# Performance work log

Measured on AMD Instinct MI355X. Metric: run time of the kernel, lower is better.

The kernel has to match this reference:

```python
import jax, jax.numpy as jnp
import numpy as np

B, S, IN, OUT, H, M = 16, 512, 512, 512, 8, 4
HF = OUT // H  # head_feats = 64


def setup_inputs() -> dict:
    key = jax.random.key(0)
    ks = jax.random.split(key, 12)
    std = 0.02
    queries = jax.random.normal(ks[0], (B, S, IN), jnp.float32)
    keys = jax.random.normal(ks[1], (B, S, IN), jnp.float32)
    timespans = jax.random.uniform(ks[2], (B, S), jnp.float32)
    # causal mask tiled over heads*batch, matching [H*B, S, S] score shape
    attention_masks = jnp.broadcast_to(jnp.tril(jnp.ones((S, S), jnp.float32)), (H * B, S, S))
    event_marks = jax.random.uniform(ks[3], (H * B, 1, S, M), jnp.float32)
    Wq = std * jax.random.normal(ks[4], (IN, OUT), jnp.float32)
    Wk = std * jax.random.normal(ks[5], (IN, OUT), jnp.float32)
    Wv = std * jax.random.normal(ks[6], (IN, OUT), jnp.float32)
    Wt = std * jax.random.normal(ks[7], (IN, OUT), jnp.float32)
    Wi = std * jax.random.normal(ks[8], (HF + 1, M * HF), jnp.float32)  # fc_i weight
    bi = jnp.zeros((M * HF,), jnp.float32)                               # fc_i bias
    weight_i = std * jax.random.normal(ks[9], (M, HF), jnp.float32)
    scale_i = jnp.zeros((M,), jnp.float32)
    return {"queries": queries, "keys": keys, "timespans": timespans,
            "attention_masks": attention_masks, "event_marks": event_marks,
            "Wq": Wq, "Wk": Wk, "Wv": Wv, "Wt": Wt, "Wi": Wi, "bi": bi,
            "weight_i": weight_i, "scale_i": scale_i}


def reference(queries, keys, timespans, attention_masks, event_marks,
              Wq, Wk, Wv, Wt, Wi, bi, weight_i, scale_i):
    # torch's cat(chunk(X, H, dim=2), dim=0) == [B,S,H,HF] -> [H,B,S,HF] -> flat h*B+b
    def split_heads(X):
        return X.reshape(B, S, H, HF).transpose(2, 0, 1, 3)  # [H,B,S,HF]

    Q = split_heads(queries @ Wq)
    K = split_heads(keys @ Wk)
    V = split_heads(keys @ Wv)
    T = split_heads(keys @ Wt)

    scores = jnp.einsum('hbqf,hbkf->hbqk', Q, K) / jnp.sqrt(jnp.float32(OUT))
    mask = attention_masks.reshape(H, B, S, S)
    scores = jnp.where(mask == 0.0, jnp.float32(-2 ** 32 + 1), scores)
    attn = jax.nn.softmax(scores, axis=-1)  # [H,B,Sq,Sk]

    E = jnp.einsum('hbqk,hbkf->hbqf', attn, T)  # events fed to intensity net

    # --- Hawkes intensities ---
    ts = jnp.broadcast_to(timespans[None, :, :, None], (H, B, S, 1))
    mu = jax.nn.sigmoid(jnp.concatenate([E, ts], axis=-1) @ Wi + bi)  # [H,B,S,M*HF]
    mu = mu.reshape(H, B, S, M, HF)  # chunk over marks along feature dim
    scale = jnp.exp(scale_i)  # [M]
    lam = jnp.einsum('hbsmf,mf->hbsm', mu, weight_i) / scale
    lam = scale * jnp.log1p(jnp.exp(lam))  # scaled softplus, [H,B,S,M]

    # mark_inty[h,b,q,k] = sum_m lam[h,b,q,m] * event_marks[h,b,k,m]
    em = event_marks.reshape(H, B, S, M)
    mark_inty = jnp.einsum('hbqm,hbkm->hbqk', lam, em)

    out = jnp.einsum('hbqk,hbkf->hbqf', attn * mark_inty, V)
    out = out.transpose(1, 2, 0, 3).reshape(B, S, OUT) + queries[..., :OUT]
    all_mark_inty = lam.reshape(H * B, S, M)
    return out, all_mark_inty
```

## Files before the change

### kernel.cpp

```cpp
#include <hip/hip_runtime.h>
#include <math.h>

typedef __attribute__((ext_vector_type(8))) short short8;
typedef __attribute__((ext_vector_type(4))) float f32x4;

static __device__ __forceinline__ unsigned short f2bf(float f) {
  unsigned int u = __float_as_uint(f);
  u += 0x7FFFu + ((u >> 16) & 1u);
  return (unsigned short)(u >> 16);
}

static __device__ __forceinline__ void cp16(void* lds, const void* g) {
  __builtin_amdgcn_global_load_lds((const __attribute__((address_space(1))) void*)g,
                                   (__attribute__((address_space(3))) void*)lds,
                                   16, 0, 0);
}

__global__ __launch_bounds__(256) void convert_k(
    const float* __restrict__ qin, const float* __restrict__ kin,
    const float* __restrict__ Wq, const float* __restrict__ Wk,
    const float* __restrict__ Wv, const float* __restrict__ Wt,
    const float* __restrict__ Wi,
    unsigned short* __restrict__ qbf, unsigned short* __restrict__ kbf,
    unsigned short* __restrict__ Wb, unsigned short* __restrict__ WiF)
{
  __shared__ unsigned short tr[64 * 68];
  const int blk = blockIdx.x, tid = threadIdx.x;
  if (blk < 8192) {
    const float* src = (blk < 4096) ? qin : kin;
    unsigned short* dst = (blk < 4096) ? qbf : kbf;
    int i = ((blk & 4095) * 256 + tid) * 4;
    float4 v = *(const float4*)(src + i);
    ushort4 o;
    o.x = f2bf(v.x); o.y = f2bf(v.y); o.z = f2bf(v.z); o.w = f2bf(v.w);
    *(ushort4*)(dst + i) = o;
  } else if (blk < 8448) {
    int t = blk - 8192;
    int which = t >> 6, tile = t & 63;
    int r0 = (tile >> 3) << 6, c0 = (tile & 7) << 6;
    const float* W = (which == 0) ? Wq : (which == 1) ? Wk : (which == 2) ? Wv : Wt;
    const int rr = tid >> 4, cc = (tid & 15) << 2;
#pragma unroll
    for (int u = 0; u < 4; ++u) {
      int r = rr + u * 16;
      float4 v = *(const float4*)(W + (size_t)(r0 + r) * 512 + c0 + cc);
      tr[(cc + 0) * 68 + r] = f2bf(v.x);
      tr[(cc + 1) * 68 + r] = f2bf(v.y);
      tr[(cc + 2) * 68 + r] = f2bf(v.z);
      tr[(cc + 3) * 68 + r] = f2bf(v.w);
    }
    __syncthreads();
    unsigned short* dst = Wb + which * 262144;
#pragma unroll
    for (int u = 0; u < 4; ++u) {
      int c = rr + u * 16;
      ushort4 o = *(const ushort4*)&tr[c * 68 + cc];
      *(ushort4*)(dst + (size_t)(c0 + c) * 512 + r0 + cc) = o;
    }
  } else {
    int e = (blk - 8448) * 256 + tid;
    int j = e & 7, ll = (e >> 3) & 63, r = e >> 9;
    int kk = r % 3, nt = r / 3;
    int col = nt * 16 + (ll & 15);
    int k = kk * 32 + (ll >> 4) * 8 + j;
    float val = (k < 64) ? Wi[k * 256 + col] : ((k == 64) ? Wi[16384 + col] : 0.0f);
    WiF[e] = f2bf(val);
  }
}

__global__ __launch_bounds__(256) void proj_mfma(
    const unsigned short* __restrict__ qin_bf, const unsigned short* __restrict__ kin_bf,
    const unsigned short* __restrict__ Wb,
    unsigned short* __restrict__ Qg, unsigned short* __restrict__ Kg,
    unsigned short* __restrict__ Vt, unsigned short* __restrict__ Tt)
{
  const int which = blockIdx.z;
  const unsigned short* A = (which == 0) ? qin_bf : kin_bf;
  const unsigned short* W = Wb + which * 262144;
  const int row0 = blockIdx.x * 128;
  const int col0 = blockIdx.y * 128;
  const int tid = threadIdx.x;
  const int wv = tid >> 6, l = tid & 63;
  const int quad = l >> 4, lc = l & 15;
  const int wm = wv >> 1, wn = wv & 1;

  __shared__ unsigned short Asm[128 * 32];
  __shared__ unsigned short Bsm[128 * 32];

  f32x4 acc[4][4] = {};
  const int c0 = tid, c1 = tid + 256;

  for (int k0 = 0; k0 < 512; k0 += 32) {
    __syncthreads();
    cp16(&Asm[c0 * 8], A + (size_t)(row0 + (c0 >> 2)) * 512 + k0 + (c0 & 3) * 8);
    cp16(&Asm[c1 * 8], A + (size_t)(row0 + (c1 >> 2)) * 512 + k0 + (c1 & 3) * 8);
    cp16(&Bsm[c0 * 8], W + (size_t)(col0 + (c0 >> 2)) * 512 + k0 + (c0 & 3) * 8);
    cp16(&Bsm[c1 * 8], W + (size_t)(col0 + (c1 >> 2)) * 512 + k0 + (c1 & 3) * 8);
    __syncthreads();
    short8 a[4], b[4];
#pragma unroll
    for (int mi = 0; mi < 4; ++mi)
      a[mi] = *(const short8*)&Asm[(wm * 64 + mi * 16 + lc) * 32 + quad * 8];
#pragma unroll
    for (int nj = 0; nj < 4; ++nj)
      b[nj] = *(const short8*)&Bsm[(wn * 64 + nj * 16 + lc) * 32 + quad * 8];
#pragma unroll
    for (int mi = 0; mi < 4; ++mi)
#pragma unroll
      for (int nj = 0; nj < 4; ++nj)
        acc[mi][nj] = __builtin_amdgcn_mfma_f32_16x16x32_bf16(a[mi], b[nj], acc[mi][nj], 0, 0, 0);
  }

  const int h = (col0 >> 6) + wn;
  const int bidx = row0 >> 9;
  const int hb = h * 16 + bidx;
  if (which < 2) {
    unsigned short* C = (which == 0) ? Qg : Kg;
    const float os = (which == 0) ? 0.044194173824159216f : 1.0f;
#pragma unroll
    for (int mi = 0; mi < 4; ++mi) {
      int sbase = (row0 & 511) + wm * 64 + mi * 16 + quad * 4;
#pragma unroll
      for (int nj = 0; nj < 4; ++nj) {
        size_t base = (size_t)hb * 32768 + (size_t)sbase * 64 + nj * 16 + lc;
#pragma unroll
        for (int reg = 0; reg < 4; ++reg)
          C[base + (size_t)reg * 64] = f2bf(acc[mi][nj][reg] * os);
      }
    }
  } else {
    unsigned short* C = (which == 2) ? Vt : Tt;
    unsigned short* scr = wn ? Bsm : Asm;
    const int sb = (row0 & 511) + wm * 64;
    __syncthreads();
#pragma unroll
    for (int round = 0; round < 2; ++round) {
      if (wm == round) {
#pragma unroll
        for (int mi = 0; mi < 4; ++mi)
#pragma unroll
          for (int nj = 0; nj < 4; ++nj)
#pragma unroll
            for (int reg = 0; reg < 4; ++reg) {
              int f = nj * 16 + lc, s = mi * 16 + quad * 4 + reg;
              int g = (s >> 3) ^ (f & 7);
              scr[f * 64 + g * 8 + (s & 7)] = f2bf(acc[mi][nj][reg]);
            }
#pragma unroll
        for (int it = 0; it < 8; ++it) {
          int fl = it * 8 + (l >> 3);
          int gg = (l & 7) ^ (fl & 7);
          short8 v = *(const short8*)&scr[fl * 64 + gg * 8];
          *(short8*)(C + (size_t)hb * 32768 + (size_t)fl * 512 + sb + (l & 7) * 8) = v;
        }
      }
      __syncthreads();
    }
  }
}

__global__ __launch_bounds__(256, 2) void attn_fused(
    const unsigned short* __restrict__ Qg, const unsigned short* __restrict__ Kg,
    const unsigned short* __restrict__ Vtg, const unsigned short* __restrict__ Ttg,
    const unsigned short* __restrict__ WiF,
    const float* __restrict__ bi, const float* __restrict__ wim,
    const float* __restrict__ sci, const float* __restrict__ tsp,
    const float* __restrict__ em, const float* __restrict__ queries,
    float* __restrict__ out, float* __restrict__ lamout)
{
  const int hb = blockIdx.x;
  const int y = blockIdx.y;
  const int qb = (y == 0) ? 3 : (y == 1) ? 2 : (y == 2) ? 0 : 1;
  const int q0 = qb << 7;
  const int kts = 2 * qb + 2;
  const int tid = threadIdx.x, wv = tid >> 6, l = tid & 63;
  const int quad = l >> 4, lc = l & 15;
  const int xg = lc & 7;

  __shared__ unsigned short Qs[8192];
  __shared__ unsigned short Ks[2][4096];
  __shared__ unsigned short TVs[2][4096];
  __shared__ unsigned short Wl[4][3072];
  __shared__ float emS[2][256];

  const int e1 = tid + 256;
  const int sr0 = tid >> 3, sg0 = (tid & 7) ^ (sr0 & 7);
  const int sr1 = e1 >> 3,  sg1 = (e1 & 7) ^ (sr1 & 7);
  const int sqk0 = sr0 * 64 + sg0 * 8,  sqk1 = sr1 * 64 + sg1 * 8;
  const int stv0 = sr0 * 512 + sg0 * 8, stv1 = sr1 * 512 + sg1 * 8;

  const unsigned short* KgB = Kg + (size_t)hb * 32768;
  const unsigned short* TgB = Ttg + (size_t)hb * 32768;
  const unsigned short* VgB = Vtg + (size_t)hb * 32768;

  const unsigned short* Qbase = Qg + (size_t)hb * 32768 + q0 * 64;
#pragma unroll
  for (int u = 0; u < 4; ++u) {
    int e = tid + u * 256;
    int r = e >> 3, g = (e & 7) ^ (r & 7);
    cp16(&Qs[e * 8], Qbase + r * 64 + g * 8);
  }
  cp16(&Ks[0][tid * 8], KgB + sqk0);
  cp16(&Ks[0][e1 * 8], KgB + sqk1);
  cp16(&TVs[0][tid * 8], TgB + stv0);
  cp16(&TVs[0][e1 * 8], TgB + stv1);
  __syncthreads();

  short8 aq[2][2];
#pragma unroll
  for (int rt = 0; rt < 2; ++rt)
#pragma unroll
    for (int kk = 0; kk < 2; ++kk)
      aq[rt][kk] = *(const short8*)&Qs[(wv * 32 + rt * 16 + lc) * 64 + ((kk * 4 + quad) ^ xg) * 8];

  f32x4 Eacc[2][4] = {};
  float lsum[2][4] = {};

  for (int kt = 0; kt < kts; ++kt) {
    const int cur = kt & 1, nxt = cur ^ 1;
    const int k0 = kt << 6;
    if (kt + 1 < kts) {
      const int k1 = (kt + 1) << 6;
      cp16(&Ks[nxt][tid * 8], KgB + k1 * 64 + sqk0);
      cp16(&Ks[nxt][e1 * 8], KgB + k1 * 64 + sqk1);
      cp16(&TVs[nxt][tid * 8], TgB + k1 + stv0);
      cp16(&TVs[nxt][e1 * 8], TgB + k1 + stv1);
    }
    f32x4 sc[2][4] = {};
#pragma unroll
    for (int kk = 0; kk < 2; ++kk)
#pragma unroll
      for (int nj = 0; nj < 4; ++nj) {
        short8 b = *(const short8*)&Ks[cur][(nj * 16 + lc) * 64 + ((kk * 4 + quad) ^ xg) * 8];
        sc[0][nj] = __builtin_amdgcn_mfma_f32_16x16x32_bf16(aq[0][kk], b, sc[0][nj], 0, 0, 0);
        sc[1][nj] = __builtin_amdgcn_mfma_f32_16x16x32_bf16(aq[1][kk], b, sc[1][nj], 0, 0, 0);
      }
#pragma unroll
    for (int rt = 0; rt < 2; ++rt) {
      const int gq = q0 + wv * 32 + rt * 16 + quad * 4;
#pragma unroll
      for (int nj = 0; nj < 4; ++nj) {
        int col = nj * 16 + lc;
#pragma unroll
        for (int reg = 0; reg < 4; ++reg) {
          float pv = __expf(sc[rt][nj][reg]);
          if (k0 + col > gq + reg) pv = 0.0f;
          lsum[rt][reg] += pv;
          int row = rt * 16 + quad * 4 + reg;
          int gp = (nj * 2 + (lc >> 3)) ^ (row & 7);
          Wl[wv][row * 96 + gp * 8 + (lc & 7)] = f2bf(pv);
        }
      }
    }
#pragma unroll
    for (int rt = 0; rt < 2; ++rt)
#pragma unroll
      for (int kk = 0; kk < 2; ++kk) {
        short8 a = *(const short8*)&Wl[wv][(rt * 16 + lc) * 96 + ((kk * 4 + quad) ^ xg) * 8];
#pragma unroll
        for (int fj = 0; fj < 4; ++fj) {
          short8 b = *(const short8*)&TVs[cur][(fj * 16 + lc) * 64 + ((kk * 4 + quad) ^ xg) * 8];
          Eacc[rt][fj] = __builtin_amdgcn_mfma_f32_16x16x32_bf16(a, b, Eacc[rt][fj], 0, 0, 0);
        }
      }
    __syncthreads();
  }

  float inv[2][4];
#pragma unroll
  for (int rt = 0; rt < 2; ++rt)
#pragma unroll
    for (int reg = 0; reg < 4; ++reg) {
      float s = lsum[rt][reg];
#pragma unroll
      for (int off = 1; off < 16; off <<= 1) s += __shfl_xor(s, off);
      inv[rt][reg] = 1.0f / s;
    }

#pragma unroll
  for (int rt = 0; rt < 2; ++rt)
#pragma unroll
    for (int reg = 0; reg < 4; ++reg) {
      int row = rt * 16 + quad * 4 + reg;
      int gq = q0 + wv * 32 + rt * 16 + quad * 4;
      unsigned short* rp = &Wl[wv][row * 96];
#pragma unroll
      for (int fj = 0; fj < 4; ++fj) {
        int gp = (fj * 2 + (lc >> 3)) ^ (row & 7);
        rp[gp * 8 + (lc & 7)] = f2bf(Eacc[rt][fj][reg] * inv[rt][reg]);
      }
      float tsv = (lc == 0) ? tsp[(hb & 15) * 512 + gq + reg] : 0.0f;
      int gt = 8 + ((lc >> 3) ^ (row & 3));
      rp[gt * 8 + (lc & 7)] = f2bf(tsv);
      int gz = 8 + ((2 + (lc >> 3)) ^ (row & 3));
      rp[gz * 8 + (lc & 7)] = 0;
    }

  float lam4[2][4][4];
#pragma unroll
  for (int rt = 0; rt < 2; ++rt) {
    short8 ia[3];
    ia[0] = *(const short8*)&Wl[wv][(rt * 16 + lc) * 96 + ((0 + quad) ^ xg) * 8];
    ia[1] = *(const short8*)&Wl[wv][(rt * 16 + lc) * 96 + ((4 + quad) ^ xg) * 8];
    ia[2] = *(const short8*)&Wl[wv][(rt * 16 + lc) * 96 + (8 + (quad ^ (lc & 3))) * 8];
    float lac[4][4] = {};
#pragma unroll
    for (int nt = 0; nt < 16; ++nt) {
      f32x4 iacc = {};
#pragma unroll
      for (int kk = 0; kk < 3; ++kk) {
        short8 b = *(const short8*)(WiF + ((nt * 3 + kk) * 64 + l) * 8);
        iacc = __builtin_amdgcn_mfma_f32_16x16x32_bf16(ia[kk], b, iacc, 0, 0, 0);
      }
      float bvv = bi[nt * 16 + lc];
      float wmv = wim[nt * 16 + lc];
#pragma unroll
      for (int reg = 0; reg < 4; ++reg) {
        float mu = 1.0f / (1.0f + __expf(-(iacc[reg] + bvv)));
        lac[reg][nt >> 2] += mu * wmv;
      }
    }
#pragma unroll
    for (int m = 0; m < 4; ++m) {
      float scv = __expf(sci[m]);
#pragma unroll
      for (int reg = 0; reg < 4; ++reg) {
        float s = lac[reg][m];
#pragma unroll
        for (int off = 1; off < 16; off <<= 1) s += __shfl_xor(s, off);
        float z = s / scv;
        float sp = (z > 20.0f) ? z : log1pf(__expf(z));
        lam4[rt][reg][m] = scv * sp;
      }
    }
    if (lc < 4) {
      int gq = q0 + wv * 32 + rt * 16 + quad * 4;
#pragma unroll
      for (int reg = 0; reg < 4; ++reg) {
        float v = (lc == 0) ? lam4[rt][reg][0] : (lc == 1) ? lam4[rt][reg][1]
                : (lc == 2) ? lam4[rt][reg][2] : lam4[rt][reg][3];
        lamout[((size_t)hb * 512 + gq + reg) * 4 + lc] = v;
      }
    }
#pragma unroll
    for (int reg = 0; reg < 4; ++reg)
#pragma unroll
      for (int m = 0; m < 4; ++m)
        lam4[rt][reg][m] *= inv[rt][reg];
  }

  cp16(&Ks[0][tid * 8], KgB + sqk0);
  cp16(&Ks[0][e1 * 8], KgB + sqk1);
  cp16(&TVs[0][tid * 8], VgB + stv0);
  cp16(&TVs[0][e1 * 8], VgB + stv1);
  emS[0][tid] = em[(size_t)hb * 2048 + tid];
  __syncthreads();

  f32x4 Oacc[2][4] = {};
  for (int kt = 0; kt < kts; ++kt) {
    const int cur = kt & 1, nxt = cur ^ 1;
    const int k0 = kt << 6;
    if (kt + 1 < kts) {
      const int k1 = (kt + 1) << 6;
      cp16(&Ks[nxt][tid * 8], KgB + k1 * 64 + sqk0);
      cp16(&Ks[nxt][e1 * 8], KgB + k1 * 64 + sqk1);
      cp16(&TVs[nxt][tid * 8], VgB + k1 + stv0);
      cp16(&TVs[nxt][e1 * 8], VgB + k1 + stv1);
      emS[nxt][tid] = em[(size_t)hb * 2048 + k1 * 4 + tid];
    }
    f32x4 sc[2][4] = {};
#pragma unroll
    for (int kk = 0; kk < 2; ++kk)
#pragma unroll
      for (int nj = 0; nj < 4; ++nj) {
        short8 b = *(const short8*)&Ks[cur][(nj * 16 + lc) * 64 + ((kk * 4 + quad) ^ xg) * 8];
        sc[0][nj] = __builtin_amdgcn_mfma_f32_16x16x32_bf16(aq[0][kk], b, sc[0][nj], 0, 0, 0);
        sc[1][nj] = __builtin_amdgcn_mfma_f32_16x16x32_bf16(aq[1][kk], b, sc[1][nj], 0, 0, 0);
      }
#pragma unroll
    for (int rt = 0; rt < 2; ++rt) {
      const int gq = q0 + wv * 32 + rt * 16 + quad * 4;
#pragma unroll
      for (int nj = 0; nj < 4; ++nj) {
        int col = nj * 16 + lc;
        float4 emv = *(const float4*)&emS[cur][col * 4];
#pragma unroll
        for (int reg = 0; reg < 4; ++reg) {
          float pv = __expf(sc[rt][nj][reg]);
          if (k0 + col > gq + reg) pv = 0.0f;
          float mk = lam4[rt][reg][0] * emv.x + lam4[rt][reg][1] * emv.y +
                     lam4[rt][reg][2] * emv.z + lam4[rt][reg][3] * emv.w;
          int row = rt * 16 + quad * 4 + reg;
          int gp = (nj * 2 + (lc >> 3)) ^ (row & 7);
          Wl[wv][row * 96 + gp * 8 + (lc & 7)] = f2bf(pv * mk);
        }
      }
    }
#pragma unroll
    for (int rt = 0; rt < 2; ++rt)
#pragma unroll
      for (int kk = 0; kk < 2; ++kk) {
        short8 a = *(const short8*)&Wl[wv][(rt * 16 + lc) * 96 + ((kk * 4 + quad) ^ xg) * 8];
#pragma unroll
        for (int fj = 0; fj < 4; ++fj) {
          short8 b = *(const short8*)&TVs[cur][(fj * 16 + lc) * 64 + ((kk * 4 + quad) ^ xg) * 8];
          Oacc[rt][fj] = __builtin_amdgcn_mfma_f32_16x16x32_bf16(a, b, Oacc[rt][fj], 0, 0, 0);
        }
      }
    __syncthreads();
  }

  const int h = hb >> 4, bidx = hb & 15;
#pragma unroll
  for (int rt = 0; rt < 2; ++rt) {
    const int gq = q0 + wv * 32 + rt * 16 + quad * 4;
#pragma unroll
    for (int reg = 0; reg < 4; ++reg) {
      size_t o = (size_t)bidx * 262144 + (size_t)(gq + reg) * 512 + h * 64 + lc;
#pragma unroll
      for (int fj = 0; fj < 4; ++fj)
        out[o + fj * 16] = Oacc[rt][fj][reg] + queries[o + fj * 16];
    }
  }
}

extern "C" void kernel_launch(void* const* d_in, const int* in_sizes, int n_in,
                              void* d_out, int out_size, void* d_ws, size_t ws_size,
                              hipStream_t stream)
{
  (void)in_sizes; (void)n_in; (void)out_size; (void)ws_size;
  const float* queries = (const float*)d_in[0];
  const float* keys    = (const float*)d_in[1];
  const float* tsp     = (const float*)d_in[2];
  const float* em      = (const float*)d_in[4];
  const float* Wq      = (const float*)d_in[5];
  const float* Wk      = (const float*)d_in[6];
  const float* Wv      = (const float*)d_in[7];
  const float* Wt      = (const float*)d_in[8];
  const float* Wi      = (const float*)d_in[9];
  const float* bi      = (const float*)d_in[10];
  const float* wim     = (const float*)d_in[11];
  const float* sci     = (const float*)d_in[12];
  float* out = (float*)d_out;

  char* w = (char*)d_ws;
  unsigned short* Qg     = (unsigned short*)(w + 0);
  unsigned short* Kg     = (unsigned short*)(w + 8388608);
  unsigned short* Vt     = (unsigned short*)(w + 16777216);
  unsigned short* Tt     = (unsigned short*)(w + 25165824);
  unsigned short* qin_bf = (unsigned short*)(w + 33554432);
  unsigned short* kin_bf = (unsigned short*)(w + 41943040);
  unsigned short* Wb     = (unsigned short*)(w + 50331648);
  unsigned short* WiF    = (unsigned short*)(w + 52428800);

  convert_k<<<8544, 256, 0, stream>>>(queries, keys, Wq, Wk, Wv, Wt, Wi,
                                      qin_bf, kin_bf, Wb, WiF);
  proj_mfma<<<dim3(64, 4, 4), 256, 0, stream>>>(qin_bf, kin_bf, Wb, Qg, Kg, Vt, Tt);
  attn_fused<<<dim3(128, 4), 256, 0, stream>>>(Qg, Kg, Vt, Tt, WiF, bi, wim, sci,
                                               tsp, em, queries, out,
                                               out + 4194304);
}
```

Measured before the change: 313.1 us.

## Fuse input bf16 conversion into projection GEMM and cache softmax probabilities in registers

```diff
diff --git a/kernel.cpp b/kernel.cpp
--- a/kernel.cpp
+++ b/kernel.cpp
@@ -17,26 +17,15 @@
 }
 
 __global__ __launch_bounds__(256) void convert_k(
-    const float* __restrict__ qin, const float* __restrict__ kin,
     const float* __restrict__ Wq, const float* __restrict__ Wk,
     const float* __restrict__ Wv, const float* __restrict__ Wt,
     const float* __restrict__ Wi,
-    unsigned short* __restrict__ qbf, unsigned short* __restrict__ kbf,
     unsigned short* __restrict__ Wb, unsigned short* __restrict__ WiF)
 {
   __shared__ unsigned short tr[64 * 68];
   const int blk = blockIdx.x, tid = threadIdx.x;
-  if (blk < 8192) {
-    const float* src = (blk < 4096) ? qin : kin;
-    unsigned short* dst = (blk < 4096) ? qbf : kbf;
-    int i = ((blk & 4095) * 256 + tid) * 4;
-    float4 v = *(const float4*)(src + i);
-    ushort4 o;
-    o.x = f2bf(v.x); o.y = f2bf(v.y); o.z = f2bf(v.z); o.w = f2bf(v.w);
-    *(ushort4*)(dst + i) = o;
-  } else if (blk < 8448) {
-    int t = blk - 8192;
-    int which = t >> 6, tile = t & 63;
+  if (blk < 256) {
+    int which = blk >> 6, tile = blk & 63;
     int r0 = (tile >> 3) << 6, c0 = (tile & 7) << 6;
     const float* W = (which == 0) ? Wq : (which == 1) ? Wk : (which == 2) ? Wv : Wt;
     const int rr = tid >> 4, cc = (tid & 15) << 2;
@@ -58,7 +47,7 @@
       *(ushort4*)(dst + (size_t)(c0 + c) * 512 + r0 + cc) = o;
     }
   } else {
-    int e = (blk - 8448) * 256 + tid;
+    int e = (blk - 256) * 256 + tid;
     int j = e & 7, ll = (e >> 3) & 63, r = e >> 9;
     int kk = r % 3, nt = r / 3;
     int col = nt * 16 + (ll & 15);
@@ -69,13 +58,13 @@
 }
 
 __global__ __launch_bounds__(256) void proj_mfma(
-    const unsigned short* __restrict__ qin_bf, const unsigned short* __restrict__ kin_bf,
+    const float* __restrict__ qin, const float* __restrict__ kin,
     const unsigned short* __restrict__ Wb,
     unsigned short* __restrict__ Qg, unsigned short* __restrict__ Kg,
     unsigned short* __restrict__ Vt, unsigned short* __restrict__ Tt)
 {
   const int which = blockIdx.z;
-  const unsigned short* A = (which == 0) ? qin_bf : kin_bf;
+  const float* A = (which == 0) ? qin : kin;
   const unsigned short* W = Wb + which * 262144;
   const int row0 = blockIdx.x * 128;
   const int col0 = blockIdx.y * 128;
@@ -84,31 +73,62 @@
   const int quad = l >> 4, lc = l & 15;
   const int wm = wv >> 1, wn = wv & 1;
 
-  __shared__ unsigned short Asm[128 * 32];
-  __shared__ unsigned short Bsm[128 * 32];
-
+  __shared__ unsigned short Asm[2][128 * 32];
+  __shared__ unsigned short Bsm[2][128 * 32];
+
+  const int e2 = tid + 256;
+  const int br0 = tid >> 2, bg0 = (tid & 3) ^ (br0 & 3);
+  const int br1 = e2 >> 2,  bg1 = (e2 & 3) ^ (br1 & 3);
   f32x4 acc[4][4] = {};
-  const int c0 = tid, c1 = tid + 256;
-
-  for (int k0 = 0; k0 < 512; k0 += 32) {
-    __syncthreads();
-    cp16(&Asm[c0 * 8], A + (size_t)(row0 + (c0 >> 2)) * 512 + k0 + (c0 & 3) * 8);
-    cp16(&Asm[c1 * 8], A + (size_t)(row0 + (c1 >> 2)) * 512 + k0 + (c1 & 3) * 8);
-    cp16(&Bsm[c0 * 8], W + (size_t)(col0 + (c0 >> 2)) * 512 + k0 + (c0 & 3) * 8);
-    cp16(&Bsm[c1 * 8], W + (size_t)(col0 + (c1 >> 2)) * 512 + k0 + (c1 & 3) * 8);
-    __syncthreads();
+
+  cp16(&Bsm[0][tid * 8], W + (size_t)(col0 + br0) * 512 + bg0 * 8);
+  cp16(&Bsm[0][e2 * 8], W + (size_t)(col0 + br1) * 512 + bg1 * 8);
+#pragma unroll
+  for (int u = 0; u < 4; ++u) {
+    int i = tid + u * 256, r = i >> 3, c4 = i & 7;
+    float4 v = *(const float4*)(A + (size_t)(row0 + r) * 512 + c4 * 4);
+    ushort4 o;
+    o.x = f2bf(v.x); o.y = f2bf(v.y); o.z = f2bf(v.z); o.w = f2bf(v.w);
+    *(ushort4*)&Asm[0][r * 32 + (((c4 >> 1) ^ (r & 3)) << 3) + ((c4 & 1) << 2)] = o;
+  }
+  __syncthreads();
+
+  const int xk = lc & 3;
+  for (int ks = 0; ks < 16; ++ks) {
+    const int cur = ks & 1, nxt = cur ^ 1;
+    float4 av[4];
+    if (ks < 15) {
+      const int k1 = (ks + 1) << 5;
+      cp16(&Bsm[nxt][tid * 8], W + (size_t)(col0 + br0) * 512 + k1 + bg0 * 8);
+      cp16(&Bsm[nxt][e2 * 8], W + (size_t)(col0 + br1) * 512 + k1 + bg1 * 8);
+#pragma unroll
+      for (int u = 0; u < 4; ++u) {
+        int i = tid + u * 256, r = i >> 3, c4 = i & 7;
+        av[u] = *(const float4*)(A + (size_t)(row0 + r) * 512 + k1 + c4 * 4);
+      }
+    }
     short8 a[4], b[4];
 #pragma unroll
     for (int mi = 0; mi < 4; ++mi)
-      a[mi] = *(const short8*)&Asm[(wm * 64 + mi * 16 + lc) * 32 + quad * 8];
+      a[mi] = *(const short8*)&Asm[cur][(wm * 64 + mi * 16 + lc) * 32 + ((quad ^ xk) << 3)];
 #pragma unroll
     for (int nj = 0; nj < 4; ++nj)
-      b[nj] = *(const short8*)&Bsm[(wn * 64 + nj * 16 + lc) * 32 + quad * 8];
+      b[nj] = *(const short8*)&Bsm[cur][(wn * 64 + nj * 16 + lc) * 32 + ((quad ^ xk) << 3)];
 #pragma unroll
     for (int mi = 0; mi < 4; ++mi)
 #pragma unroll
       for (int nj = 0; nj < 4; ++nj)
         acc[mi][nj] = __builtin_amdgcn_mfma_f32_16x16x32_bf16(a[mi], b[nj], acc[mi][nj], 0, 0, 0);
+    if (ks < 15) {
+#pragma unroll
+      for (int u = 0; u < 4; ++u) {
+        int i = tid + u * 256, r = i >> 3, c4 = i & 7;
+        ushort4 o;
+        o.x = f2bf(av[u].x); o.y = f2bf(av[u].y); o.z = f2bf(av[u].z); o.w = f2bf(av[u].w);
+        *(ushort4*)&Asm[nxt][r * 32 + (((c4 >> 1) ^ (r & 3)) << 3) + ((c4 & 1) << 2)] = o;
+      }
+    }
+    __syncthreads();
   }
 
   const int h = (col0 >> 6) + wn;
@@ -130,7 +150,7 @@
     }
   } else {
     unsigned short* C = (which == 2) ? Vt : Tt;
-    unsigned short* scr = wn ? Bsm : Asm;
+    unsigned short* scr = wn ? Bsm[0] : Asm[0];
     const int sb = (row0 & 511) + wm * 64;
     __syncthreads();
 #pragma unroll
@@ -215,8 +235,11 @@
 
   f32x4 Eacc[2][4] = {};
   float lsum[2][4] = {};
-
-  for (int kt = 0; kt < kts; ++kt) {
+  unsigned int Pc[8][16];
+
+#pragma unroll
+  for (int kt = 0; kt < 8; ++kt) {
+    if (kt >= kts) continue;
     const int cur = kt & 1, nxt = cur ^ 1;
     const int k0 = kt << 6;
     if (kt + 1 < kts) {
@@ -241,15 +264,19 @@
 #pragma unroll
       for (int nj = 0; nj < 4; ++nj) {
         int col = nj * 16 + lc;
+        unsigned short pb[4];
 #pragma unroll
         for (int reg = 0; reg < 4; ++reg) {
           float pv = __expf(sc[rt][nj][reg]);
           if (k0 + col > gq + reg) pv = 0.0f;
           lsum[rt][reg] += pv;
+          pb[reg] = f2bf(pv);
           int row = rt * 16 + quad * 4 + reg;
           int gp = (nj * 2 + (lc >> 3)) ^ (row & 7);
-          Wl[wv][row * 96 + gp * 8 + (lc & 7)] = f2bf(pv);
+          Wl[wv][row * 96 + gp * 8 + (lc & 7)] = pb[reg];
         }
+        Pc[kt][(rt * 4 + nj) * 2 + 0] = (unsigned int)pb[0] | ((unsigned int)pb[1] << 16);
+        Pc[kt][(rt * 4 + nj) * 2 + 1] = (unsigned int)pb[2] | ((unsigned int)pb[3] << 16);
       }
     }
 #pragma unroll
@@ -276,6 +303,10 @@
       for (int off = 1; off < 16; off <<= 1) s += __shfl_xor(s, off);
       inv[rt][reg] = 1.0f / s;
     }
+
+  cp16(&Ks[0][tid * 8], VgB + stv0);
+  cp16(&Ks[0][e1 * 8], VgB + stv1);
+  emS[0][tid] = em[(size_t)hb * 2048 + tid];
 
 #pragma unroll
   for (int rt = 0; rt < 2; ++rt)
@@ -348,51 +379,39 @@
       for (int m = 0; m < 4; ++m)
         lam4[rt][reg][m] *= inv[rt][reg];
   }
-
-  cp16(&Ks[0][tid * 8], KgB + sqk0);
-  cp16(&Ks[0][e1 * 8], KgB + sqk1);
-  cp16(&TVs[0][tid * 8], VgB + stv0);
-  cp16(&TVs[0][e1 * 8], VgB + stv1);
-  emS[0][tid] = em[(size_t)hb * 2048 + tid];
   __syncthreads();
 
   f32x4 Oacc[2][4] = {};
-  for (int kt = 0; kt < kts; ++kt) {
+#pragma unroll
+  for (int kt = 0; kt < 8; ++kt) {
+    if (kt >= kts) continue;
     const int cur = kt & 1, nxt = cur ^ 1;
-    const int k0 = kt << 6;
     if (kt + 1 < kts) {
       const int k1 = (kt + 1) << 6;
-      cp16(&Ks[nxt][tid * 8], KgB + k1 * 64 + sqk0);
-      cp16(&Ks[nxt][e1 * 8], KgB + k1 * 64 + sqk1);
-      cp16(&TVs[nxt][tid * 8], VgB + k1 + stv0);
-      cp16(&TVs[nxt][e1 * 8], VgB + k1 + stv1);
+      cp16(&Ks[nxt][tid * 8], VgB + k1 + stv0);
+      cp16(&Ks[nxt][e1 * 8], VgB + k1 + stv1);
       emS[nxt][tid] = em[(size_t)hb * 2048 + k1 * 4 + tid];
     }
-    f32x4 sc[2][4] = {};
-#pragma unroll
-    for (int kk = 0; kk < 2; ++kk)
-#pragma unroll
-      for (int nj = 0; nj < 4; ++nj) {
-        short8 b = *(const short8*)&Ks[cur][(nj * 16 + lc) * 64 + ((kk * 4 + quad) ^ xg) * 8];
-        sc[0][nj] = __builtin_amdgcn_mfma_f32_16x16x32_bf16(aq[0][kk], b, sc[0][nj], 0, 0, 0);
-        sc[1][nj] = __builtin_amdgcn_mfma_f32_16x16x32_bf16(aq[1][kk], b, sc[1][nj], 0, 0, 0);
-      }
 #pragma unroll
     for (int rt = 0; rt < 2; ++rt) {
-      const int gq = q0 + wv * 32 + rt * 16 + quad * 4;
 #pragma unroll
       for (int nj = 0; nj < 4; ++nj) {
         int col = nj * 16 + lc;
         float4 emv = *(const float4*)&emS[cur][col * 4];
+        unsigned int u0 = Pc[kt][(rt * 4 + nj) * 2 + 0];
+        unsigned int u1 = Pc[kt][(rt * 4 + nj) * 2 + 1];
+        float p[4];
+        p[0] = __uint_as_float(u0 << 16);
+        p[1] = __uint_as_float(u0 & 0xFFFF0000u);
+        p[2] = __uint_as_float(u1 << 16);
+        p[3] = __uint_as_float(u1 & 0xFFFF0000u);
 #pragma unroll
         for (int reg = 0; reg < 4; ++reg) {
-          float pv = __expf(sc[rt][nj][reg]);
-          if (k0 + col > gq + reg) pv = 0.0f;
           float mk = lam4[rt][reg][0] * emv.x + lam4[rt][reg][1] * emv.y +
                      lam4[rt][reg][2] * emv.z + lam4[rt][reg][3] * emv.w;
           int row = rt * 16 + quad * 4 + reg;
           int gp = (nj * 2 + (lc >> 3)) ^ (row & 7);
-          Wl[wv][row * 96 + gp * 8 + (lc & 7)] = f2bf(pv * mk);
+          Wl[wv][row * 96 + gp * 8 + (lc & 7)] = f2bf(p[reg] * mk);
         }
       }
     }
@@ -403,7 +422,7 @@
         short8 a = *(const short8*)&Wl[wv][(rt * 16 + lc) * 96 + ((kk * 4 + quad) ^ xg) * 8];
 #pragma unroll
         for (int fj = 0; fj < 4; ++fj) {
-          short8 b = *(const short8*)&TVs[cur][(fj * 16 + lc) * 64 + ((kk * 4 + quad) ^ xg) * 8];
+          short8 b = *(const short8*)&Ks[cur][(fj * 16 + lc) * 64 + ((kk * 4 + quad) ^ xg) * 8];
           Oacc[rt][fj] = __builtin_amdgcn_mfma_f32_16x16x32_bf16(a, b, Oacc[rt][fj], 0, 0, 0);
         }
       }
@@ -444,18 +463,15 @@
   float* out = (float*)d_out;
 
   char* w = (char*)d_ws;
-  unsigned short* Qg     = (unsigned short*)(w + 0);
-  unsigned short* Kg     = (unsigned short*)(w + 8388608);
-  unsigned short* Vt     = (unsigned short*)(w + 16777216);
-  unsigned short* Tt     = (unsigned short*)(w + 25165824);
-  unsigned short* qin_bf = (unsigned short*)(w + 33554432);
-  unsigned short* kin_bf = (unsigned short*)(w + 41943040);
-  unsigned short* Wb     = (unsigned short*)(w + 50331648);
-  unsigned short* WiF    = (unsigned short*)(w + 52428800);
-
-  convert_k<<<8544, 256, 0, stream>>>(queries, keys, Wq, Wk, Wv, Wt, Wi,
-                                      qin_bf, kin_bf, Wb, WiF);
-  proj_mfma<<<dim3(64, 4, 4), 256, 0, stream>>>(qin_bf, kin_bf, Wb, Qg, Kg, Vt, Tt);
+  unsigned short* Qg  = (unsigned short*)(w + 0);
+  unsigned short* Kg  = (unsigned short*)(w + 8388608);
+  unsigned short* Vt  = (unsigned short*)(w + 16777216);
+  unsigned short* Tt  = (unsigned short*)(w + 25165824);
+  unsigned short* Wb  = (unsigned short*)(w + 33554432);
+  unsigned short* WiF = (unsigned short*)(w + 35651584);
+
+  convert_k<<<352, 256, 0, stream>>>(Wq, Wk, Wv, Wt, Wi, Wb, WiF);
+  proj_mfma<<<dim3(64, 4, 4), 256, 0, stream>>>(queries, keys, Wb, Qg, Kg, Vt, Tt);
   attn_fused<<<dim3(128, 4), 256, 0, stream>>>(Qg, Kg, Vt, Tt, WiF, bi, wim, sci,
                                                tsp, em, queries, out,
                                                out + 4194304);
```

New measurement: 322.9 us. +3.1%, slower.
